# Performance work log

Measured on AMD Instinct MI355X. Metric: run time of the kernel, lower is better.

Reference implementation:

```python
import jax, jax.numpy as jnp
import numpy as np

B, D, M, C = 8192, 2048, 8, 1000

def setup_inputs() -> dict:
    key = jax.random.key(0)
    k1, k2, k3, k4, k5 = jax.random.split(key, 5)
    scale = 1.0 / np.sqrt(D)
    return {
        "x": jax.random.normal(k1, (B, D), dtype=jnp.float32),
        "model_weights": jax.random.normal(k2, (M, D, C), dtype=jnp.float32) * scale,
        "model_bias": jax.random.normal(k3, (M, C), dtype=jnp.float32) * 0.01,
        "resnet_weight": jax.random.normal(k4, (D, M * C), dtype=jnp.float32) * scale,
        "resnet_bias": jax.random.normal(k5, (M * C,), dtype=jnp.float32) * 0.01,
    }

def reference(x, model_weights, model_bias, resnet_weight, resnet_bias):
    # Per-submodel logits: [B, M, C]
    outputs = jnp.einsum("bd,mdc->bmc", x, model_weights) + model_bias[None, :, :]
    # Fusion weights from the weighting network: [B, M, C]
    w = (x @ resnet_weight + resnet_bias).reshape(x.shape[0], model_weights.shape[0], model_weights.shape[2])
    # Fused weighted sum over models (replaces the triple Python loop): [B, C]
    result = jnp.sum(outputs * w, axis=1)
    return result
```

## Files before the change

### kernel.cpp

```cpp
#include <hip/hip_runtime.h>
#include <hip/hip_bf16.h>
#include <stdint.h>

#define BDIM 8192
#define DDIM 2048
#define MDIM 8
#define CDIM 1000
#define CPAD 1024
#define NPAD 8192

typedef __attribute__((ext_vector_type(8))) short bf16x8;
typedef __attribute__((ext_vector_type(4))) float f32x4;

__device__ __forceinline__ unsigned short f2bf(float f) {
    union { float f; unsigned u; } v; v.f = f;
    unsigned r = v.u + 0x7fffu + ((v.u >> 16) & 1u);
    return (unsigned short)(r >> 16);
}

__device__ __forceinline__ void gl_lds16(const void* g, void* l) {
    __builtin_amdgcn_global_load_lds(
        (const __attribute__((address_space(1))) void*)g,
        (__attribute__((address_space(3))) void*)l,
        16, 0, 0);
}

__global__ void cast_x_kernel(const float4* __restrict__ x, ushort* __restrict__ xb) {
    int i = blockIdx.x * blockDim.x + threadIdx.x;
    float4 v = x[i];
    ushort4 o;
    o.x = f2bf(v.x); o.y = f2bf(v.y); o.z = f2bf(v.z); o.w = f2bf(v.w);
    *(ushort4*)&xb[(size_t)i * 4] = o;
}

__global__ void prep_w(const float* __restrict__ MW, ushort* __restrict__ wb) {
    __shared__ float tile[32][33];
    int m  = blockIdx.z;
    int c0 = blockIdx.x * 32;
    int d0 = blockIdx.y * 32;
    int tx = threadIdx.x, ty = threadIdx.y;
    const float* src = MW + (size_t)m * DDIM * CDIM;
#pragma unroll
    for (int i = 0; i < 4; i++) {
        int d = d0 + ty + i * 8;
        int c = c0 + tx;
        tile[ty + i * 8][tx] = (c < CDIM) ? src[(size_t)d * CDIM + c] : 0.f;
    }
    __syncthreads();
#pragma unroll
    for (int i = 0; i < 4; i++) {
        int c = c0 + ty + i * 8;
        int d = d0 + tx;
        wb[(size_t)(c * 8 + m) * DDIM + d] = f2bf(tile[tx][ty + i * 8]);
    }
}

__global__ void prep_r(const float* __restrict__ R, ushort* __restrict__ rb) {
    __shared__ float tile[32][33];
    int m  = blockIdx.z;
    int c0 = blockIdx.x * 32;
    int d0 = blockIdx.y * 32;
    int tx = threadIdx.x, ty = threadIdx.y;
#pragma unroll
    for (int i = 0; i < 4; i++) {
        int d = d0 + ty + i * 8;
        int c = c0 + tx;
        tile[ty + i * 8][tx] = (c < CDIM) ? R[(size_t)d * (MDIM * CDIM) + m * CDIM + c] : 0.f;
    }
    __syncthreads();
#pragma unroll
    for (int i = 0; i < 4; i++) {
        int c = c0 + ty + i * 8;
        int d = d0 + tx;
        rb[(size_t)(c * 8 + m) * DDIM + d] = f2bf(tile[tx][ty + i * 8]);
    }
}

__global__ void prep_bias(const float* __restrict__ mb, const float* __restrict__ rbv,
                          float* __restrict__ mb2, float* __restrict__ rb2) {
    int n = blockIdx.x * 256 + threadIdx.x;
    int c = n >> 3, m = n & 7;
    mb2[n] = (c < CDIM) ? mb[m * CDIM + c] : 0.f;
    rb2[n] = (c < CDIM) ? rbv[m * CDIM + c] : 0.f;
}

#define BM 256
#define BN 128
#define BK 64
#define NT (DDIM / BK)

#define STAGE(G, L) do {                                                       \
    _Pragma("unroll")                                                          \
    for (int it_ = 0; it_ < 2; ++it_) {                                        \
        int ci_ = it_ * 512 + tid;                                             \
        int r_ = ci_ >> 3, cc_ = ci_ & 7;                                      \
        gl_lds16((G) + (size_t)r_ * DDIM + (size_t)((cc_ ^ (r_ & 7)) << 3),    \
                 (L) + (size_t)(it_ * 512 + wbase) * 8);                       \
    }                                                                          \
} while (0)

#define LDA(AC, H) do {                                                        \
    _Pragma("unroll")                                                          \
    for (int i_ = 0; i_ < 4; i_++)                                             \
    _Pragma("unroll")                                                          \
    for (int kh_ = 0; kh_ < 2; kh_++) {                                        \
        int row_ = (H) * 128 + wm * 64 + i_ * 16 + (lane & 15);                \
        int cc_ = kh_ * 4 + (lane >> 4);                                       \
        af[i_][kh_] = *(const bf16x8*)&(AC)[row_ * BK + ((cc_ ^ (row_ & 7)) << 3)]; \
    }                                                                          \
} while (0)

#define LDB(BS, BF) do {                                                       \
    _Pragma("unroll")                                                          \
    for (int j_ = 0; j_ < 2; j_++)                                             \
    _Pragma("unroll")                                                          \
    for (int kh_ = 0; kh_ < 2; kh_++) {                                        \
        int row_ = wn * 32 + j_ * 16 + (lane & 15);                            \
        int cc_ = kh_ * 4 + (lane >> 4);                                       \
        BF[j_][kh_] = *(const bf16x8*)&(BS)[row_ * BK + ((cc_ ^ (row_ & 7)) << 3)]; \
    }                                                                          \
} while (0)

#define MM(ACC, H, BF) do {                                                    \
    __builtin_amdgcn_s_setprio(1);                                             \
    _Pragma("unroll")                                                          \
    for (int i_ = 0; i_ < 4; i_++)                                             \
    _Pragma("unroll")                                                          \
    for (int j_ = 0; j_ < 2; j_++)                                             \
    _Pragma("unroll")                                                          \
    for (int kh_ = 0; kh_ < 2; kh_++)                                          \
        ACC[(H) * 4 + i_][j_] = __builtin_amdgcn_mfma_f32_16x16x32_bf16(       \
            af[i_][kh_], BF[j_][kh_], ACC[(H) * 4 + i_][j_], 0, 0, 0);         \
    __builtin_amdgcn_s_setprio(0);                                             \
} while (0)

#define FENCE() asm volatile("" ::: "memory")
#define BARRIER() do { FENCE(); __builtin_amdgcn_s_barrier(); FENCE(); } while (0)
#define WAITV(N) asm volatile("s_waitcnt vmcnt(" #N ")" ::: "memory")

__global__ __launch_bounds__(512, 2) void gemm_fused(
    const ushort* __restrict__ xb, const ushort* __restrict__ wb,
    const ushort* __restrict__ rb,
    const float* __restrict__ mb2, const float* __restrict__ rb2,
    float* __restrict__ out) {
    __shared__ ushort As[2][BM * BK];
    __shared__ ushort B1s[2][BN * BK];
    __shared__ ushort B2s[2][BN * BK];

    int tid   = threadIdx.x;
    int lane  = tid & 63;
    int wid   = tid >> 6;
    int wm    = wid >> 2;
    int wn    = wid & 3;
    int wbase = tid & ~63;

    int wg = blockIdx.x;
    int wgs = (wg & 7) * 256 + (wg >> 3);
    int tile_m = wgs >> 6;
    int tile_n = wgs & 63;
    int brow = tile_m * BM;
    int bn0  = tile_n * BN;

    const ushort* xg  = xb + (size_t)brow * DDIM;
    const ushort* w1g = wb + (size_t)bn0 * DDIM;
    const ushort* w2g = rb + (size_t)bn0 * DDIM;

    f32x4 acc1[8][2] = {};
    f32x4 acc2[8][2] = {};
    bf16x8 af[4][2], bf1[2][2], bf2[2][2];

    STAGE(xg,              As[0]);
    STAGE(w1g,             B1s[0]);
    STAGE(w2g,             B2s[0]);
    STAGE(xg + 128 * DDIM, As[0] + 128 * BK);
    WAITV(4);
    BARRIER();

#pragma unroll 2
    for (int t = 0; t < NT; ++t) {
        int buf = t & 1;
        ushort* Ac  = As[buf];
        ushort* B1c = B1s[buf];
        ushort* B2c = B2s[buf];
        ushort* An  = As[buf ^ 1];
        ushort* B1n = B1s[buf ^ 1];
        ushort* B2n = B2s[buf ^ 1];
        const int kn = (t + 1) * BK;

        LDA(Ac, 0);
        LDB(B1c, bf1);
        STAGE(xg + kn,             An);
        STAGE(w1g + kn,            B1n);
        STAGE(w2g + kn,            B2n);
        STAGE(xg + 128 * DDIM + kn, An + 128 * BK);
        MM(acc1, 0, bf1);
        WAITV(8);
        BARRIER();

        LDB(B2c, bf2);
        MM(acc2, 0, bf2);
        LDA(Ac, 1);
        MM(acc1, 1, bf1);
        MM(acc2, 1, bf2);
        WAITV(4);
        BARRIER();
    }
    WAITV(0);

#pragma unroll
    for (int j = 0; j < 2; j++) {
        int np = bn0 + wn * 32 + j * 16 + (lane & 15);
        float bb1 = mb2[np];
        float bb2 = rb2[np];
        int c = tile_n * 16 + wn * 4 + j * 2 + ((lane >> 3) & 1);
#pragma unroll
        for (int rf = 0; rf < 8; rf++) {
#pragma unroll
            for (int r = 0; r < 4; r++) {
                float p = (acc1[rf][j][r] + bb1) * (acc2[rf][j][r] + bb2);
                p += __shfl_xor(p, 1);
                p += __shfl_xor(p, 2);
                p += __shfl_xor(p, 4);
                if ((lane & 7) == 0 && c < CDIM) {
                    int row = brow + (rf >> 2) * 128 + wm * 64 + (rf & 3) * 16
                              + ((lane >> 4) << 2) + r;
                    out[(size_t)row * CDIM + c] = p;
                }
            }
        }
    }
}

extern "C" void kernel_launch(void* const* d_in, const int* in_sizes, int n_in,
                              void* d_out, int out_size, void* d_ws, size_t ws_size,
                              hipStream_t stream) {
    const float* x   = (const float*)d_in[0];
    const float* mw  = (const float*)d_in[1];
    const float* mb  = (const float*)d_in[2];
    const float* rw  = (const float*)d_in[3];
    const float* rbv = (const float*)d_in[4];
    float* out = (float*)d_out;

    char* ws = (char*)d_ws;
    ushort* xb  = (ushort*)ws;
    ushort* wb  = (ushort*)(ws + (size_t)33554432);
    ushort* rb  = (ushort*)(ws + (size_t)67108864);
    float*  mb2 = (float*)(ws + (size_t)100663296);
    float*  rb2 = (float*)(ws + (size_t)100696064);

    cast_x_kernel<<<BDIM * DDIM / (256 * 4), 256, 0, stream>>>((const float4*)x, xb);
    prep_w<<<dim3(CPAD / 32, DDIM / 32, MDIM), dim3(32, 8), 0, stream>>>(mw, wb);
    prep_r<<<dim3(CPAD / 32, DDIM / 32, MDIM), dim3(32, 8), 0, stream>>>(rw, rb);
    prep_bias<<<NPAD / 256, 256, 0, stream>>>(mb, rbv, mb2, rb2);

    gemm_fused<<<dim3((BDIM / BM) * (NPAD / BN)), 512, 0, stream>>>(xb, wb, rb, mb2, rb2, out);
}
```

Baseline: 604.9 us.

## Restructure GEMM main loop into four-phase ping-pong with split-K LDS reads

Splits each K-tile iteration into four barrier-separated phases. Each phase loads half of the A/B fragments from LDS, issues one global-to-LDS stage, and runs a block of MFMAs under raised priority. The top A half for tile t+2 is prefetched into the current buffer early, so global loads spread more evenly across the iteration. The aim is better overlap between LDS reads, global loads and MFMA work, at the cost of more barriers per iteration and subtle buffer-reuse hazards.

```diff
diff --git a/kernel.cpp b/kernel.cpp
--- a/kernel.cpp
+++ b/kernel.cpp
@@ -99,44 +99,38 @@
     }                                                                          \
 } while (0)
 
-#define LDA(AC, H) do {                                                        \
+#define LDA_K(AC, H, KH) do {                                                  \
+    _Pragma("unroll")                                                          \
+    for (int i_ = 0; i_ < 4; i_++) {                                           \
+        int row_ = (H) * 128 + wm * 64 + i_ * 16 + (lane & 15);                \
+        int cc_ = (KH) * 4 + (lane >> 4);                                      \
+        af[i_][KH] = *(const bf16x8*)&(AC)[row_ * BK + ((cc_ ^ (row_ & 7)) << 3)]; \
+    }                                                                          \
+} while (0)
+
+#define LDB_K(BS, BF, KH) do {                                                 \
+    _Pragma("unroll")                                                          \
+    for (int j_ = 0; j_ < 2; j_++) {                                           \
+        int row_ = wn * 32 + j_ * 16 + (lane & 15);                            \
+        int cc_ = (KH) * 4 + (lane >> 4);                                      \
+        BF[j_][KH] = *(const bf16x8*)&(BS)[row_ * BK + ((cc_ ^ (row_ & 7)) << 3)]; \
+    }                                                                          \
+} while (0)
+
+#define MMK(ACC, H, BF, KH) do {                                               \
     _Pragma("unroll")                                                          \
     for (int i_ = 0; i_ < 4; i_++)                                             \
     _Pragma("unroll")                                                          \
-    for (int kh_ = 0; kh_ < 2; kh_++) {                                        \
-        int row_ = (H) * 128 + wm * 64 + i_ * 16 + (lane & 15);                \
-        int cc_ = kh_ * 4 + (lane >> 4);                                       \
-        af[i_][kh_] = *(const bf16x8*)&(AC)[row_ * BK + ((cc_ ^ (row_ & 7)) << 3)]; \
-    }                                                                          \
-} while (0)
-
-#define LDB(BS, BF) do {                                                       \
-    _Pragma("unroll")                                                          \
     for (int j_ = 0; j_ < 2; j_++)                                             \
-    _Pragma("unroll")                                                          \
-    for (int kh_ = 0; kh_ < 2; kh_++) {                                        \
-        int row_ = wn * 32 + j_ * 16 + (lane & 15);                            \
-        int cc_ = kh_ * 4 + (lane >> 4);                                       \
-        BF[j_][kh_] = *(const bf16x8*)&(BS)[row_ * BK + ((cc_ ^ (row_ & 7)) << 3)]; \
-    }                                                                          \
-} while (0)
-
-#define MM(ACC, H, BF) do {                                                    \
-    __builtin_amdgcn_s_setprio(1);                                             \
-    _Pragma("unroll")                                                          \
-    for (int i_ = 0; i_ < 4; i_++)                                             \
-    _Pragma("unroll")                                                          \
-    for (int j_ = 0; j_ < 2; j_++)                                             \
-    _Pragma("unroll")                                                          \
-    for (int kh_ = 0; kh_ < 2; kh_++)                                          \
         ACC[(H) * 4 + i_][j_] = __builtin_amdgcn_mfma_f32_16x16x32_bf16(       \
-            af[i_][kh_], BF[j_][kh_], ACC[(H) * 4 + i_][j_], 0, 0, 0);         \
-    __builtin_amdgcn_s_setprio(0);                                             \
+            af[i_][KH], BF[j_][KH], ACC[(H) * 4 + i_][j_], 0, 0, 0);           \
 } while (0)
 
 #define FENCE() asm volatile("" ::: "memory")
 #define BARRIER() do { FENCE(); __builtin_amdgcn_s_barrier(); FENCE(); } while (0)
 #define WAITV(N) asm volatile("s_waitcnt vmcnt(" #N ")" ::: "memory")
+#define SP1() __builtin_amdgcn_s_setprio(1)
+#define SP0() __builtin_amdgcn_s_setprio(0)
 
 __global__ __launch_bounds__(512, 2) void gemm_fused(
     const ushort* __restrict__ xb, const ushort* __restrict__ wb,
@@ -169,10 +163,11 @@
     f32x4 acc2[8][2] = {};
     bf16x8 af[4][2], bf1[2][2], bf2[2][2];
 
-    STAGE(xg,              As[0]);
-    STAGE(w1g,             B1s[0]);
-    STAGE(w2g,             B2s[0]);
-    STAGE(xg + 128 * DDIM, As[0] + 128 * BK);
+    STAGE(xg,               As[0]);
+    STAGE(w1g,              B1s[0]);
+    STAGE(w2g,              B2s[0]);
+    STAGE(xg + 128 * DDIM,  As[0] + 128 * BK);
+    STAGE(xg + BK,          As[1]);
     WAITV(4);
     BARRIER();
 
@@ -185,24 +180,39 @@
         ushort* An  = As[buf ^ 1];
         ushort* B1n = B1s[buf ^ 1];
         ushort* B2n = B2s[buf ^ 1];
-        const int kn = (t + 1) * BK;
-
-        LDA(Ac, 0);
-        LDB(B1c, bf1);
-        STAGE(xg + kn,             An);
-        STAGE(w1g + kn,            B1n);
-        STAGE(w2g + kn,            B2n);
+        const int kn  = (t + 1) * BK;
+        const int kn2 = (t + 2) * BK;
+
+        LDA_K(Ac, 0, 0);
+        LDB_K(B1c, bf1, 0);
+        LDB_K(B2c, bf2, 0);
+        STAGE(w1g + kn, B1n);
+        BARRIER();
+        SP1(); MMK(acc1, 0, bf1, 0); MMK(acc2, 0, bf2, 0); SP0();
+        BARRIER();
+
+        LDA_K(Ac, 0, 1);
+        LDB_K(B1c, bf1, 1);
+        LDB_K(B2c, bf2, 1);
+        STAGE(w2g + kn, B2n);
+        SP1();
+        WAITV(4);
+        BARRIER();
+        MMK(acc1, 0, bf1, 1); MMK(acc2, 0, bf2, 1); SP0();
+        BARRIER();
+
+        LDA_K(Ac, 1, 0);
+        LDA_K(Ac, 1, 1);
         STAGE(xg + 128 * DDIM + kn, An + 128 * BK);
-        MM(acc1, 0, bf1);
-        WAITV(8);
-        BARRIER();
-
-        LDB(B2c, bf2);
-        MM(acc2, 0, bf2);
-        LDA(Ac, 1);
-        MM(acc1, 1, bf1);
-        MM(acc2, 1, bf2);
+        BARRIER();
+        SP1(); MMK(acc1, 1, bf1, 0); MMK(acc1, 1, bf1, 1); SP0();
+        BARRIER();
+
+        STAGE(xg + kn2, Ac);
+        BARRIER();
+        SP1(); MMK(acc2, 1, bf2, 0); MMK(acc2, 1, bf2, 1);
         WAITV(4);
+        SP0();
         BARRIER();
     }
     WAITV(0);
```

Measured after the change: 592.8 us. 1.02x faster.
